# Optimization experiments

Hardware: AMD Instinct MI355X
Metric: run time of the kernel (lower is better)

Reference implementation:

```python
import jax, jax.numpy as jnp
import numpy as np
from jax import lax


def _conv(x, w, b):
    out = lax.conv_general_dilated(x, w, (1, 1), [(0, 0), (0, 0)],
                                   dimension_numbers=('NCHW', 'OIHW', 'NCHW'))
    return out + b[None, :, None, None]


def _bn(x, g, b, eps=1e-5):
    # BatchNorm2d in training mode: biased batch statistics over (N,H,W)
    m = jnp.mean(x, axis=(0, 2, 3), keepdims=True)
    v = jnp.var(x, axis=(0, 2, 3), keepdims=True)
    return (x - m) * lax.rsqrt(v + eps) * g[None, :, None, None] + b[None, :, None, None]


def _maxpool2(x):
    return lax.reduce_window(x, -jnp.inf, lax.max, (1, 1, 2, 2), (1, 1, 2, 2), 'VALID')


def _topk_mask(x, k):
    # TopK module: keep the k largest-|.| channels per (b,h,w), zero the rest.
    a = jnp.abs(x)
    kth = lax.top_k(jnp.moveaxis(a, 1, -1), k)[0][..., -1]  # [B,H,W] k-th largest |x|
    return x * (a >= kth[:, None, :, :]).astype(x.dtype)


def _embiggen(x):
    # im2col 3x3 stride 1 valid, flattened channel-major (c, kh, kw) like
    # patch.contiguous().view(B,-1) in the torch loop, but fully vectorized.
    B, C, H, W = x.shape
    Ho, Wo = H - 2, W - 2
    patches = jnp.stack([x[:, :, i:i + Ho, j:j + Wo]
                         for i in range(3) for j in range(3)], axis=2)  # [B,C,9,Ho,Wo]
    return patches.reshape(B, C * 9, Ho, Wo)


def setup_inputs() -> dict:
    key = jax.random.key(0)
    ks = jax.random.split(key, 40)
    it = iter(range(40))

    def w(shape):
        fan_in = int(np.prod(shape[1:]))
        return (jax.random.normal(ks[next(it)], shape, jnp.float32)
                / np.float32(np.sqrt(fan_in)))

    def bias(n):
        return jax.random.normal(ks[next(it)], (n,), jnp.float32) * 0.01

    def gamma(n):
        return jax.random.uniform(ks[next(it)], (n,), jnp.float32, 0.5, 1.5)

    inp = {}
    inp['x'] = jax.random.normal(ks[next(it)], (256, 3, 32, 32), jnp.float32)
    inp['enc_w'] = w((256, 3, 3, 3)); inp['enc_b'] = bias(256)
    inp['dec_w'] = w((27, 256, 1, 1)); inp['dec_b'] = bias(27)
    inp['red_w'] = w((64, 256, 1, 1)); inp['red_b'] = bias(64)
    inp['bn1_g'] = gamma(64); inp['bn1_b'] = bias(64)
    inp['conv1_w'] = w((96, 64, 3, 3)); inp['conv1_b'] = bias(96)
    inp['bn2_g'] = gamma(96); inp['bn2_b'] = bias(96)
    inp['conv2_w'] = w((128, 96, 3, 3)); inp['conv2_b'] = bias(128)
    inp['bn3_g'] = gamma(128); inp['bn3_b'] = bias(128)
    inp['conv3_w'] = w((160, 128, 3, 3)); inp['conv3_b'] = bias(160)
    inp['bn4_g'] = gamma(160); inp['bn4_b'] = bias(160)
    inp['conv4_w'] = w((192, 160, 3, 3)); inp['conv4_b'] = bias(192)
    inp['bn5_g'] = gamma(192); inp['bn5_b'] = bias(192)
    inp['conv5_w'] = w((256, 192, 3, 3)); inp['conv5_b'] = bias(256)
    inp['bnc_g'] = gamma(256); inp['bnc_b'] = bias(256)
    inp['fc_w'] = w((100, 1024)); inp['fc_b'] = bias(100)
    inp['k'] = 32  # round(64 / k_div=2)
    return inp


def reference(x, enc_w, enc_b, dec_w, dec_b, red_w, red_b,
              bn1_g, bn1_b, conv1_w, conv1_b,
              bn2_g, bn2_b, conv2_w, conv2_b,
              bn3_g, bn3_b, conv3_w, conv3_b,
              bn4_g, bn4_b, conv4_w, conv4_b,
              bn5_g, bn5_b, conv5_w, conv5_b,
              bnc_g, bnc_b, fc_w, fc_b, k):
    # SparseCodingLayer_First (encoder+topk computed once; torch recomputes identically)
    s = _topk_mask(_conv(x, enc_w, enc_b), k)            # [B,256,30,30]
    dec = jax.nn.sigmoid(_conv(s, dec_w, dec_b))         # [B,27,30,30]
    target = lax.stop_gradient(_embiggen(x))             # detached im2col target
    aux_loss = jnp.mean((target - dec) ** 2)
    h = _conv(s, red_w, red_b)                           # [B,64,30,30]
    # Conv6 backbone
    h = _maxpool2(_conv(jax.nn.relu(_bn(h, bn1_g, bn1_b)), conv1_w, conv1_b))  # [B,96,14,14]
    h = _conv(jax.nn.relu(_bn(h, bn2_g, bn2_b)), conv2_w, conv2_b)             # [B,128,12,12]
    h = _conv(jax.nn.relu(_bn(h, bn3_g, bn3_b)), conv3_w, conv3_b)             # [B,160,10,10]
    h = _maxpool2(_conv(jax.nn.relu(_bn(h, bn4_g, bn4_b)), conv4_w, conv4_b))  # [B,192,4,4]
    h = _conv(jax.nn.relu(_bn(h, bn5_g, bn5_b)), conv5_w, conv5_b)             # [B,256,2,2]
    feat = lax.stop_gradient(h)  # usecase == 'pretrain': features detached
    f = _bn(feat, bnc_g, bnc_b).reshape(feat.shape[0], -1)  # [B,1024]
    logits = f @ fc_w.T + fc_b                               # [B,100]
    preds = jnp.argmax(logits, axis=1)
    return logits, preds, aux_loss
```

## Files before the change

### kernel.cpp

```cpp
#include <hip/hip_runtime.h>

#define DEV_INLINE __device__ __forceinline__
typedef unsigned long long ull;
typedef unsigned int u32;
typedef unsigned short u16;
typedef __attribute__((ext_vector_type(8))) short short8v;
typedef __attribute__((ext_vector_type(4))) float f32x4;

DEV_INLINE u32 rne16(float f){
  u32 u = __float_as_uint(f);
  return (u + 0x7fffu + ((u>>16)&1u)) >> 16;
}
DEV_INLINE u32 packsplit(float a){
  u32 h = rne16(a);
  float hf = __uint_as_float(h<<16);
  u32 l = rne16(a - hf);
  return h | (l<<16);
}
DEV_INLINE float unpackv(u32 w){
  return __uint_as_float(w<<16) + __uint_as_float(w & 0xffff0000u);
}

__global__ void prep_all(const float* __restrict__ enc_w, float* __restrict__ encTg,
                         const float* __restrict__ dec_w, float* __restrict__ decT,
                         const float* __restrict__ red_w, float* __restrict__ redT,
                         const float* __restrict__ fc_w,  float* __restrict__ fcT,
                         const float* __restrict__ c1w, u16* __restrict__ W1h, u16* __restrict__ W1l,
                         const float* __restrict__ c2w, u16* __restrict__ W2h, u16* __restrict__ W2l,
                         const float* __restrict__ c3w, u16* __restrict__ W3h, u16* __restrict__ W3l,
                         const float* __restrict__ c4w, u16* __restrict__ W4h, u16* __restrict__ W4l,
                         const float* __restrict__ c5w, u16* __restrict__ W5h, u16* __restrict__ W5l)
{
  const int b = blockIdx.x, t = threadIdx.x;
  auto t2 = [&](const float* A, float* AT, int R, int C, int base){
    int i = (b-base)*256 + t; if (i < R*C){ int r=i%R, c=i/R; AT[i] = A[r*C+c]; }
  };
  auto pk = [&](const float* W, u16* wh, u16* wl, int CIN, int COUT, int base){
    int TPI = CIN/32;
    int eid = (b-base)*256 + t;
    if (eid >= 9*TPI*COUT*32) return;
    int kl = eid & 31;
    int rem = eid >> 5;
    int co = rem % COUT, ks = rem / COUT;
    int tap = ks/TPI, cib = (ks - tap*TPI)*32;
    float w = W[((size_t)(co*CIN + cib + kl))*9 + tap];
    u32 h = rne16(w);
    float hf = __uint_as_float(h<<16);
    u32 l = rne16(w - hf);
    wh[(size_t)rem*32 + kl] = (u16)h;
    wl[(size_t)rem*32 + kl] = (u16)l;
  };
  if      (b < 27)   t2(enc_w, encTg, 256, 27, 0);
  else if (b < 54)   t2(dec_w, decT, 27, 256, 27);
  else if (b < 118)  t2(red_w, redT, 64, 256, 54);
  else if (b < 518)  t2(fc_w,  fcT, 100, 1024, 118);
  else if (b < 734)  pk(c1w, W1h, W1l, 64, 96, 518);
  else if (b < 1166) pk(c2w, W2h, W2l, 96, 128, 734);
  else if (b < 1886) pk(c3w, W3h, W3l, 128, 160, 1166);
  else if (b < 2966) pk(c4w, W4h, W4l, 160, 192, 1886);
  else               pk(c5w, W5h, W5l, 192, 256, 2966);
}

__global__ __launch_bounds__(256, 4) void stage_a1(
    const float* __restrict__ encTg, const float* __restrict__ enc_b,
    const float* __restrict__ x, const int* __restrict__ kp,
    float* __restrict__ svg_v, unsigned char* __restrict__ svg_i)
{
  __shared__ float  rows[9*32];
  __shared__ float  svf[30*33];
  __shared__ unsigned char svi[30*33];

  const int t = threadIdx.x, oh = blockIdx.x, b = blockIdx.y;
  const int k = __builtin_amdgcn_readfirstlane(*kp);
  const int wid = t>>6, lane = t&63;
  const float4* encW4 = (const float4*)encTg;

  for (int e=t; e<288; e+=256){
    int ci = e/96, r = (e/32)%3, xx = e&31;
    rows[(ci*3+r)*32+xx] = x[((b*3+ci)*32 + (oh+r))*32 + xx];
  }
  for (int e=t; e<990; e+=256){ svf[e]=0.f; svi[e]=0; }
  __syncthreads();

  const float4 eb = ((const float4*)enc_b)[lane];

  auto cnt4 = [&](unsigned c, unsigned u0, unsigned u1, unsigned u2, unsigned u3)->int{
    return __popcll(__ballot(u0>=c)) + __popcll(__ballot(u1>=c))
         + __popcll(__ballot(u2>=c)) + __popcll(__ballot(u3>=c));
  };
  auto compact = [&](float v0,float v1,float v2,float v3,
                     unsigned u0,unsigned u1,unsigned u2,unsigned u3,
                     unsigned th, int pi){
    bool k0=u0>=th, k1=u1>=th, k2=u2>=th, k3=u3>=th;
    ull B0=__ballot(k0), B1=__ballot(k1), B2=__ballot(k2), B3=__ballot(k3);
    ull below=(1ull<<lane)-1ull;
    int n0=__popcll(B0), n1=__popcll(B1), n2=__popcll(B2);
    int o0=__popcll(B0&below);
    int o1=n0+__popcll(B1&below);
    int o2=n0+n1+__popcll(B2&below);
    int o3=n0+n1+n2+__popcll(B3&below);
    float* sf = &svf[pi*33]; unsigned char* si = &svi[pi*33];
    if (k0&&o0<32){ sf[o0]=v0; si[o0]=(unsigned char)(4*lane+0); }
    if (k1&&o1<32){ sf[o1]=v1; si[o1]=(unsigned char)(4*lane+1); }
    if (k2&&o2<32){ sf[o2]=v2; si[o2]=(unsigned char)(4*lane+2); }
    if (k3&&o3<32){ sf[o3]=v3; si[o3]=(unsigned char)(4*lane+3); }
  };

  for (int it=0; it<4; ++it){
    const int pr = wid*4 + it;
    if (pr >= 15) break;
    const int ow0 = 2*pr;

    float a0=eb.x,a1=eb.y,a2=eb.z,a3=eb.w;
    float c0=eb.x,c1=eb.y,c2=eb.z,c3=eb.w;
    #pragma unroll
    for (int ci=0; ci<3; ++ci)
      #pragma unroll
      for (int i=0;i<3;++i){
        const int rbase = (ci*3+i)*32 + ow0;
        float p0 = rows[rbase+0], p1 = rows[rbase+1];
        float p2 = rows[rbase+2], p3 = rows[rbase+3];
        float4 w0 = encW4[(ci*9+i*3+0)*64 + lane];
        float4 w1 = encW4[(ci*9+i*3+1)*64 + lane];
        float4 w2 = encW4[(ci*9+i*3+2)*64 + lane];
        a0=fmaf(w0.x,p0,a0); a1=fmaf(w0.y,p0,a1); a2=fmaf(w0.z,p0,a2); a3=fmaf(w0.w,p0,a3);
        c0=fmaf(w0.x,p1,c0); c1=fmaf(w0.y,p1,c1); c2=fmaf(w0.z,p1,c2); c3=fmaf(w0.w,p1,c3);
        a0=fmaf(w1.x,p1,a0); a1=fmaf(w1.y,p1,a1); a2=fmaf(w1.z,p1,a2); a3=fmaf(w1.w,p1,a3);
        c0=fmaf(w1.x,p2,c0); c1=fmaf(w1.y,p2,c1); c2=fmaf(w1.z,p2,c2); c3=fmaf(w1.w,p2,c3);
        a0=fmaf(w2.x,p2,a0); a1=fmaf(w2.y,p2,a1); a2=fmaf(w2.z,p2,a2); a3=fmaf(w2.w,p2,a3);
        c0=fmaf(w2.x,p3,c0); c1=fmaf(w2.y,p3,c1); c2=fmaf(w2.z,p3,c2); c3=fmaf(w2.w,p3,c3);
      }

    unsigned A0=__float_as_uint(a0)&0x7fffffffu, A1=__float_as_uint(a1)&0x7fffffffu;
    unsigned A2=__float_as_uint(a2)&0x7fffffffu, A3=__float_as_uint(a3)&0x7fffffffu;
    unsigned C0=__float_as_uint(c0)&0x7fffffffu, C1=__float_as_uint(c1)&0x7fffffffu;
    unsigned C2=__float_as_uint(c2)&0x7fffffffu, C3=__float_as_uint(c3)&0x7fffffffu;

    unsigned thA=0, thB=0;
    int dA=0, dB=0;
    for (int bit=30; bit>=0; --bit){
      if (!dA){
        unsigned c = thA | (1u<<bit);
        int n = cnt4(c,A0,A1,A2,A3);
        if (n>=k) thA=c;
        if (n==k) dA=1;
      }
      if (!dB){
        unsigned c = thB | (1u<<bit);
        int n = cnt4(c,C0,C1,C2,C3);
        if (n>=k) thB=c;
        if (n==k) dB=1;
      }
      if (dA & dB) break;
    }

    compact(a0,a1,a2,a3, A0,A1,A2,A3, thA, ow0);
    compact(c0,c1,c2,c3, C0,C1,C2,C3, thB, ow0+1);
  }
  __syncthreads();

  const size_t gbase = (size_t)b*900 + (size_t)oh*30;
  for (int e=t; e<960; e+=256){
    int jj = e/30, pi = e - jj*30;
    svg_v[(size_t)jj*230400 + gbase + pi] = svf[pi*33+jj];
    svg_i[(size_t)jj*230400 + gbase + pi] = svi[pi*33+jj];
  }
}

__global__ __launch_bounds__(256, 2) void stage_a2(
    const float* __restrict__ svg_v, const unsigned char* __restrict__ svg_i,
    const float* __restrict__ decT, const float* __restrict__ dec_b,
    const float* __restrict__ x, float* __restrict__ auxp)
{
  __shared__ __align__(16) float decl[256*28];
  __shared__ float redbuf[256];
  const int t = threadIdx.x;
  for (int e=t; e<6912; e+=256){
    int r = e/27, o = e - r*27;
    decl[r*28+o] = decT[e];
  }
  __syncthreads();

  const int pos = blockIdx.x*256 + t;
  const int b = pos/900, rem = pos - b*900;
  const int oh = rem/30, ow = rem - (rem/30)*30;

  float d[27];
  #pragma unroll
  for (int o=0;o<27;++o) d[o] = dec_b[o];
  for (int jj=0; jj<32; ++jj){
    float v  = svg_v[(size_t)jj*230400 + pos];
    int  idx = (int)svg_i[(size_t)jj*230400 + pos];
    const float4* wr4 = (const float4*)(decl + idx*28);
    float4 w0=wr4[0], w1=wr4[1], w2=wr4[2], w3=wr4[3], w4=wr4[4], w5=wr4[5], w6=wr4[6];
    d[0]=fmaf(v,w0.x,d[0]);  d[1]=fmaf(v,w0.y,d[1]);  d[2]=fmaf(v,w0.z,d[2]);  d[3]=fmaf(v,w0.w,d[3]);
    d[4]=fmaf(v,w1.x,d[4]);  d[5]=fmaf(v,w1.y,d[5]);  d[6]=fmaf(v,w1.z,d[6]);  d[7]=fmaf(v,w1.w,d[7]);
    d[8]=fmaf(v,w2.x,d[8]);  d[9]=fmaf(v,w2.y,d[9]);  d[10]=fmaf(v,w2.z,d[10]); d[11]=fmaf(v,w2.w,d[11]);
    d[12]=fmaf(v,w3.x,d[12]); d[13]=fmaf(v,w3.y,d[13]); d[14]=fmaf(v,w3.z,d[14]); d[15]=fmaf(v,w3.w,d[15]);
    d[16]=fmaf(v,w4.x,d[16]); d[17]=fmaf(v,w4.y,d[17]); d[18]=fmaf(v,w4.z,d[18]); d[19]=fmaf(v,w4.w,d[19]);
    d[20]=fmaf(v,w5.x,d[20]); d[21]=fmaf(v,w5.y,d[21]); d[22]=fmaf(v,w5.z,d[22]); d[23]=fmaf(v,w5.w,d[23]);
    d[24]=fmaf(v,w6.x,d[24]); d[25]=fmaf(v,w6.y,d[25]); d[26]=fmaf(v,w6.z,d[26]);
  }
  float acc = 0.f;
  #pragma unroll
  for (int o=0;o<27;++o){
    int ci = o/9, r2 = (o - ci*9)/3, c2 = o%3;
    float tg = x[((b*3+ci)*32 + (oh+r2))*32 + (ow+c2)];
    float dv = 1.f/(1.f + __expf(-d[o]));
    float df = tg - dv;
    acc = fmaf(df, df, acc);
  }
  redbuf[t]=acc; __syncthreads();
  for (int off=128; off; off>>=1){ if (t<off) redbuf[t]+=redbuf[t+off]; __syncthreads(); }
  if (t==0) auxp[blockIdx.x] = redbuf[0];
}

__global__ __launch_bounds__(256) void stage_a3p2(
    const float* __restrict__ svg_v, const unsigned char* __restrict__ svg_i,
    const float* __restrict__ redT, const float* __restrict__ red_b,
    u32* __restrict__ x1p, float* __restrict__ psum1, float* __restrict__ psq1)
{
  __shared__ __align__(16) float redl[256*68];
  __shared__ u32   obuf[256*65];
  const int t = threadIdx.x;
  for (int e=t; e<16384; e+=256) redl[(e>>6)*68 + (e&63)] = redT[e];
  __syncthreads();

  const int pos = blockIdx.x*256 + t;

  float v[32]; int a[32];
  #pragma unroll
  for (int j=0;j<32;++j) v[j] = svg_v[(size_t)j*230400 + pos];
  #pragma unroll
  for (int j=0;j<32;++j) a[j] = (int)svg_i[(size_t)j*230400 + pos]*17;

  const float4* redl4 = (const float4*)redl;
  #pragma unroll 2
  for (int ocb=0; ocb<16; ++ocb){
    float s0 = red_b[4*ocb+0], s1 = red_b[4*ocb+1];
    float s2 = red_b[4*ocb+2], s3 = red_b[4*ocb+3];
    #pragma unroll
    for (int j=0;j<32;++j){
      float4 w = redl4[a[j] + ocb];
      s0 = fmaf(v[j], w.x, s0); s1 = fmaf(v[j], w.y, s1);
      s2 = fmaf(v[j], w.z, s2); s3 = fmaf(v[j], w.w, s3);
    }
    obuf[t*65 + 4*ocb+0] = packsplit(s0);
    obuf[t*65 + 4*ocb+1] = packsplit(s1);
    obuf[t*65 + 4*ocb+2] = packsplit(s2);
    obuf[t*65 + 4*ocb+3] = packsplit(s3);
  }
  __syncthreads();

  const size_t base = (size_t)blockIdx.x*16384;
  float s = 0.f, q = 0.f;
  for (int e=t; e<16384; e+=256){
    u32 w = obuf[(e>>6)*65 + (e&63)];
    x1p[base + e] = w;
    float vv = unpackv(w);
    s += vv; q = fmaf(vv, vv, q);
  }
  float* ls = redl; float* lq = redl + 256;
  ls[t] = s; lq[t] = q; __syncthreads();
  if (t < 128){ ls[t] += ls[t+128]; lq[t] += lq[t+128]; } __syncthreads();
  if (t < 64){
    psum1[(size_t)blockIdx.x*64 + t] = ls[t] + ls[t+64];
    psq1 [(size_t)blockIdx.x*64 + t] = lq[t] + lq[t+64];
  }
}

__global__ __launch_bounds__(256) void bn1_final(
    const float* __restrict__ ps, const float* __restrict__ pq,
    const float* __restrict__ g, const float* __restrict__ b2,
    float* __restrict__ sc, float* __restrict__ sh)
{
  __shared__ float ls[256], lq[256];
  const int c = blockIdx.x, t = threadIdx.x;
  float s=0.f, q=0.f;
  for (int i=t; i<900; i+=256){ s += ps[(size_t)i*64+c]; q += pq[(size_t)i*64+c]; }
  ls[t]=s; lq[t]=q; __syncthreads();
  for (int off=128; off; off>>=1){
    if (t<off){ ls[t]+=ls[t+off]; lq[t]+=lq[t+off]; } __syncthreads();
  }
  if (t==0){
    constexpr float inv_n = 1.f/230400.f;
    float m = ls[0]*inv_n;
    float var = fmaf(lq[0], inv_n, -m*m);
    float rs = rsqrtf(var + 1e-5f);
    float scale = g[c]*rs;
    sc[c] = scale;
    sh[c] = fmaf(-m, scale, b2[c]);
  }
}

template<int C>
__global__ __launch_bounds__(256) void bn_finalG(
    const float* __restrict__ ps, const float* __restrict__ pq, int G,
    const float* __restrict__ g, const float* __restrict__ b2,
    float* __restrict__ sc, float* __restrict__ sh, float inv_n)
{
  __shared__ float ls[256], lq[256];
  const int c = blockIdx.x, t = threadIdx.x;
  float s=0.f, q=0.f;
  for (int i=t; i<G; i+=256){ s += ps[(size_t)i*C+c]; q += pq[(size_t)i*C+c]; }
  ls[t]=s; lq[t]=q; __syncthreads();
  for (int off=128; off; off>>=1){
    if (t<off){ ls[t]+=ls[t+off]; lq[t]+=lq[t+off]; } __syncthreads();
  }
  if (t==0){
    float m = ls[0]*inv_n;
    float var = fmaf(lq[0], inv_n, -m*m);
    float rs = rsqrtf(var + 1e-5f);
    float scale = g[c]*rs;
    sc[c] = scale;
    sh[c] = fmaf(-m, scale, b2[c]);
  }
}

template<int C>
__global__ void cvt_repack(u32* __restrict__ xp, const float* __restrict__ sc,
                           const float* __restrict__ sh, int total4){
  int i = blockIdx.x*256 + threadIdx.x;
  if (i >= total4) return;
  uint4* p = (uint4*)xp;
  uint4 w = p[i];
  int cb = (i*4) % C;
  w.x = packsplit(fmaxf(fmaf(unpackv(w.x), sc[cb+0], sh[cb+0]), 0.f));
  w.y = packsplit(fmaxf(fmaf(unpackv(w.y), sc[cb+1], sh[cb+1]), 0.f));
  w.z = packsplit(fmaxf(fmaf(unpackv(w.z), sc[cb+2], sh[cb+2]), 0.f));
  w.w = packsplit(fmaxf(fmaf(unpackv(w.w), sc[cb+3], sh[cb+3]), 0.f));
  p[i] = w;
}

template<int CIN,int COUT,int HIN,int WIN,int BM,int MW,bool POOL,bool PKOUT>
__global__ __launch_bounds__(256) void conv_mfma(
    const u32* __restrict__ xp, const u16* __restrict__ wh,
    const u16* __restrict__ wl, const float* __restrict__ bias,
    void* __restrict__ y_, float* __restrict__ psC, float* __restrict__ qsC)
{
  constexpr int HC=HIN-2, WC=WIN-2, TPI=CIN/32, KS=9*TPI, NCH=COUT/16;
  const int t = threadIdx.x, wid = t>>6, lane = t&63;
  const int p0 = blockIdx.x*BM;
  const int colg = lane>>4;
  const int col = lane&15;
  float* yf = (float*)y_;
  u32*   yp = (u32*)y_;

  const u32* Aptr[MW];
  #pragma unroll
  for (int m=0;m<MW;++m){
    int l = (wid*MW+m)*16 + col;
    int lc = l < BM ? l : BM-1;
    int p = p0 + lc;
    int b = p/(HC*WC); int rem = p - b*(HC*WC);
    int oh = rem/WC, ow = rem - (rem/WC)*WC;
    Aptr[m] = xp + ((size_t)((b*HIN+oh)*WIN+ow))*CIN + colg*8;
  }
  const size_t wb = (size_t)col*32 + colg*8;

  f32x4 acc[MW][NCH];
  #pragma unroll
  for (int m=0;m<MW;++m)
    #pragma unroll
    for (int nc=0;nc<NCH;++nc) acc[m][nc] = (f32x4){0.f,0.f,0.f,0.f};

  for (int ks=0; ks<KS; ++ks){
    const int tap = ks/TPI, cib = (ks - tap*TPI)*32;
    const int kh = tap/3, kw = tap - kh*3;
    short8v ah[MW], al[MW];
    #pragma unroll
    for (int m=0;m<MW;++m){
      const u32* ap = Aptr[m] + (kh*WIN + kw)*CIN + cib;
      uint4 qa = *(const uint4*)(ap);
      uint4 qb = *(const uint4*)(ap+4);
      ah[m][0]=(short)(qa.x&0xffffu); al[m][0]=(short)(qa.x>>16);
      ah[m][1]=(short)(qa.y&0xffffu); al[m][1]=(short)(qa.y>>16);
      ah[m][2]=(short)(qa.z&0xffffu); al[m][2]=(short)(qa.z>>16);
      ah[m][3]=(short)(qa.w&0xffffu); al[m][3]=(short)(qa.w>>16);
      ah[m][4]=(short)(qb.x&0xffffu); al[m][4]=(short)(qb.x>>16);
      ah[m][5]=(short)(qb.y&0xffffu); al[m][5]=(short)(qb.y>>16);
      ah[m][6]=(short)(qb.z&0xffffu); al[m][6]=(short)(qb.z>>16);
      ah[m][7]=(short)(qb.w&0xffffu); al[m][7]=(short)(qb.w>>16);
    }
    const u16* whp = wh + (size_t)ks*COUT*32 + wb;
    const u16* wlp = wl + (size_t)ks*COUT*32 + wb;
    #pragma unroll
    for (int nc=0;nc<NCH;++nc){
      short8v bh = *(const short8v*)(whp + nc*512);
      short8v bl = *(const short8v*)(wlp + nc*512);
      #pragma unroll
      for (int m=0;m<MW;++m){
        acc[m][nc] = __builtin_amdgcn_mfma_f32_16x16x32_bf16(ah[m], bh, acc[m][nc], 0,0,0);
        acc[m][nc] = __builtin_amdgcn_mfma_f32_16x16x32_bf16(ah[m], bl, acc[m][nc], 0,0,0);
        acc[m][nc] = __builtin_amdgcn_mfma_f32_16x16x32_bf16(al[m], bh, acc[m][nc], 0,0,0);
      }
    }
  }

  if constexpr (!POOL){
    __shared__ float ldsS[4][COUT], ldsQ[4][COUT];
    float sacc[NCH], qacc[NCH];
    #pragma unroll
    for (int nc=0;nc<NCH;++nc){ sacc[nc]=0.f; qacc[nc]=0.f; }
    #pragma unroll
    for (int m=0;m<MW;++m){
      const int lr0 = (wid*MW+m)*16 + colg*4;
      #pragma unroll
      for (int nc=0;nc<NCH;++nc){
        float bv = bias[nc*16+col];
        #pragma unroll
        for (int r=0;r<4;++r)
          if (lr0+r < BM){
            float ov = acc[m][nc][r] + bv;
            float vv;
            if constexpr (PKOUT){
              u32 w = packsplit(ov);
              yp[(size_t)(p0+lr0+r)*COUT + nc*16+col] = w;
              vv = unpackv(w);
            } else {
              yf[(size_t)(p0+lr0+r)*COUT + nc*16+col] = ov;
              vv = ov;
            }
            sacc[nc] += vv; qacc[nc] = fmaf(vv, vv, qacc[nc]);
          }
      }
    }
    #pragma unroll
    for (int nc=0;nc<NCH;++nc){
      float s_ = sacc[nc], q_ = qacc[nc];
      s_ += __shfl_xor(s_, 16); q_ += __shfl_xor(q_, 16);
      s_ += __shfl_xor(s_, 32); q_ += __shfl_xor(q_, 32);
      if (colg == 0){ ldsS[wid][nc*16+col] = s_; ldsQ[wid][nc*16+col] = q_; }
    }
    __syncthreads();
    if (t < COUT){
      psC[(size_t)blockIdx.x*COUT + t] = ldsS[0][t]+ldsS[1][t]+ldsS[2][t]+ldsS[3][t];
      qsC[(size_t)blockIdx.x*COUT + t] = ldsQ[0][t]+ldsQ[1][t]+ldsQ[2][t]+ldsQ[3][t];
    }
  } else {
    constexpr int LDC = COUT+4;
    __shared__ float lds[BM*LDC];
    #pragma unroll
    for (int m=0;m<MW;++m){
      const int lr0 = (wid*MW+m)*16 + colg*4;
      #pragma unroll
      for (int nc=0;nc<NCH;++nc){
        float bv = bias[nc*16+col];
        #pragma unroll
        for (int r=0;r<4;++r)
          if (lr0+r < BM) lds[(lr0+r)*LDC + nc*16+col] = acc[m][nc][r] + bv;
      }
    }
    __syncthreads();
    constexpr int WPO = WC/2;
    const size_t pbase = (size_t)p0/4;
    if (t < COUT){
      float s = 0.f, q = 0.f;
      for (int pl=0; pl<BM/4; ++pl){
        int poh = pl / WPO, pw = pl - poh*WPO;
        int r = (2*poh)*WC + 2*pw;
        float mx = fmaxf(fmaxf(lds[r*LDC+t],      lds[(r+1)*LDC+t]),
                         fmaxf(lds[(r+WC)*LDC+t], lds[(r+WC+1)*LDC+t]));
        float vv;
        if constexpr (PKOUT){
          u32 w = packsplit(mx);
          yp[(pbase + pl)*COUT + t] = w;
          vv = unpackv(w);
        } else {
          yf[(pbase + pl)*COUT + t] = mx;
          vv = mx;
        }
        s += vv; q = fmaf(vv, vv, q);
      }
      psC[(size_t)blockIdx.x*COUT + t] = s;
      qsC[(size_t)blockIdx.x*COUT + t] = q;
    }
  }
}

__global__ __launch_bounds__(256) void fc_kernel(
    const float* __restrict__ a5, const float* __restrict__ scale, const float* __restrict__ shift,
    const float* __restrict__ fcT, const float* __restrict__ fc_b,
    const float* __restrict__ auxp, float* __restrict__ outp)
{
  const int b = blockIdx.x, t = threadIdx.x;
  if (b == 256){
    __shared__ float s[256];
    float a=0.f;
    for (int i=t; i<900; i+=256) a += auxp[i];
    s[t]=a; __syncthreads();
    for (int off=128; off; off>>=1){ if (t<off) s[t]+=s[t+off]; __syncthreads(); }
    if (t==0) outp[25856] = s[0] / 6220800.0f;
    return;
  }
  __shared__ float f[1024];
  __shared__ float part[256];
  __shared__ float lg[128];
  for (int e=t; e<1024; e+=256){
    int c = e & 255, hw = e >> 8;
    float v = a5[b*1024 + e];
    f[c*4 + hw] = fmaf(v, scale[c], shift[c]);
  }
  __syncthreads();
  const int o = t & 127, half = t >> 7;
  float s = 0.f;
  if (o < 100){
    const float* fp = f + half*512;
    const float* wp = fcT + half*512*100 + o;
    for (int j=0;j<512;++j) s = fmaf(fp[j], wp[j*100], s);
  }
  part[t] = s; __syncthreads();
  if (t < 128){
    float logit = part[t] + part[t+128] + ((t<100)? fc_b[t] : 0.f);
    lg[t] = (t<100)? logit : -3.0e38f;
    if (t<100) outp[b*100 + t] = logit;
  }
  __syncthreads();
  if (t==0){
    float m = lg[0]; int mi = 0;
    for (int i=1;i<100;++i){ if (lg[i] > m){ m = lg[i]; mi = i; } }
    outp[25600 + b] = (float)mi;
  }
}

extern "C" void kernel_launch(void* const* d_in, const int* in_sizes, int n_in,
                              void* d_out, int out_size, void* d_ws, size_t ws_size,
                              hipStream_t stream)
{
  (void)in_sizes; (void)n_in; (void)out_size;
  const float* x     = (const float*)d_in[0];
  const float* enc_w = (const float*)d_in[1];
  const float* enc_b = (const float*)d_in[2];
  const float* dec_w = (const float*)d_in[3];
  const float* dec_b = (const float*)d_in[4];
  const float* red_w = (const float*)d_in[5];
  const float* red_b = (const float*)d_in[6];
  const float* bn1_g = (const float*)d_in[7];  const float* bn1_b = (const float*)d_in[8];
  const float* c1w   = (const float*)d_in[9];  const float* c1b   = (const float*)d_in[10];
  const float* bn2_g = (const float*)d_in[11]; const float* bn2_b = (const float*)d_in[12];
  const float* c2w   = (const float*)d_in[13]; const float* c2b   = (const float*)d_in[14];
  const float* bn3_g = (const float*)d_in[15]; const float* bn3_b = (const float*)d_in[16];
  const float* c3w   = (const float*)d_in[17]; const float* c3b   = (const float*)d_in[18];
  const float* bn4_g = (const float*)d_in[19]; const float* bn4_b = (const float*)d_in[20];
  const float* c4w   = (const float*)d_in[21]; const float* c4b   = (const float*)d_in[22];
  const float* bn5_g = (const float*)d_in[23]; const float* bn5_b = (const float*)d_in[24];
  const float* c5w   = (const float*)d_in[25]; const float* c5b   = (const float*)d_in[26];
  const float* bnc_g = (const float*)d_in[27]; const float* bnc_b = (const float*)d_in[28];
  const float* fc_w  = (const float*)d_in[29]; const float* fc_b  = (const float*)d_in[30];
  const int*   kp    = (const int*)d_in[31];
  float* out = (float*)d_out;
  float* ws  = (float*)d_ws;

  constexpr size_t OFF_ENCT = 0;
  constexpr size_t OFF_DECT = 7168;
  constexpr size_t OFF_REDT = 14336;
  constexpr size_t OFF_FCT  = 30720;
  constexpr size_t OFF_W1H = 133120, OFF_W1L = 160768;
  constexpr size_t OFF_W2H = 188416, OFF_W2L = 243712;
  constexpr size_t OFF_W3H = 299008, OFF_W3L = 391168;
  constexpr size_t OFF_W4H = 483328, OFF_W4L = 621568;
  constexpr size_t OFF_W5H = 759808, OFF_W5L = 980992;
  constexpr size_t OFF_SS1 = 1202176, OFF_SS2 = 1202304, OFF_SS3 = 1202496;
  constexpr size_t OFF_SS4 = 1202752, OFF_SS5 = 1203072, OFF_SSC = 1203456;
  constexpr size_t OFF_AUX  = 1302272;
  constexpr size_t OFF_B    = 1303296;
  constexpr size_t OFF_C    = 16048896;
  constexpr size_t OFF_P1S  = 25264896;
  constexpr size_t OFF_P1Q  = OFF_P1S + 57600;
  constexpr size_t OFF_PCS  = OFF_P1Q + 57600;
  constexpr size_t OFF_PCQ  = OFF_PCS + 172032;
  constexpr size_t TOTALF   = OFF_PCQ + 172032;
  if (ws_size < TOTALF*sizeof(float)) return;

  float* encTg = ws + OFF_ENCT;
  float* decT = ws + OFF_DECT; float* redT = ws + OFF_REDT; float* fcT = ws + OFF_FCT;
  u16* W1h = (u16*)(ws+OFF_W1H); u16* W1l = (u16*)(ws+OFF_W1L);
  u16* W2h = (u16*)(ws+OFF_W2H); u16* W2l = (u16*)(ws+OFF_W2L);
  u16* W3h = (u16*)(ws+OFF_W3H); u16* W3l = (u16*)(ws+OFF_W3L);
  u16* W4h = (u16*)(ws+OFF_W4H); u16* W4l = (u16*)(ws+OFF_W4L);
  u16* W5h = (u16*)(ws+OFF_W5H); u16* W5l = (u16*)(ws+OFF_W5L);
  float* ss1 = ws+OFF_SS1; float* ss2 = ws+OFF_SS2; float* ss3 = ws+OFF_SS3;
  float* ss4 = ws+OFF_SS4; float* ss5 = ws+OFF_SS5; float* ssc = ws+OFF_SSC;
  float* auxp = ws+OFF_AUX;
  float* psum1 = ws+OFF_P1S; float* psq1 = ws+OFF_P1Q;
  float* pcs = ws+OFF_PCS;  float* pcq = ws+OFF_PCQ;
  u32*   x1p = (u32*)(ws+OFF_B);
  u32*   y2p = (u32*)(ws+OFF_B);
  u32*   p4p = (u32*)(ws+OFF_B);
  float* svv = ws+OFF_C;
  unsigned char* svi = (unsigned char*)(ws+OFF_C+7372800);
  u32*   p1p = (u32*)(ws+OFF_C);
  u32*   y3p = (u32*)(ws+OFF_C);
  float* y5  = ws+OFF_C;

  prep_all<<<4694, 256, 0, stream>>>(enc_w, encTg, dec_w, decT, red_w, redT, fc_w, fcT,
                                     c1w, W1h, W1l, c2w, W2h, W2l, c3w, W3h, W3l,
                                     c4w, W4h, W4l, c5w, W5h, W5l);

  stage_a1<<<dim3(30,256), 256, 0, stream>>>(encTg, enc_b, x, kp, svv, svi);
  stage_a2<<<900, 256, 0, stream>>>(svv, svi, decT, dec_b, x, auxp);
  stage_a3p2<<<900, 256, 0, stream>>>(svv, svi, redT, red_b, x1p, psum1, psq1);

  bn1_final<<<64, 256, 0, stream>>>(psum1, psq1, bn1_g, bn1_b, ss1, ss1+64);
  cvt_repack<64><<<14400, 256, 0, stream>>>(x1p, ss1, ss1+64, 3686400);

  conv_mfma<64,96,30,30,112,2,true,true><<<1792, 256, 0, stream>>>(x1p, W1h, W1l, c1b, p1p, pcs, pcq);
  bn_finalG<96><<<96, 256, 0, stream>>>(pcs, pcq, 1792, bn2_g, bn2_b, ss2, ss2+96, 1.f/50176.f);
  cvt_repack<96><<<(1204224+255)/256, 256, 0, stream>>>(p1p, ss2, ss2+96, 1204224);

  conv_mfma<96,128,14,14,192,3,false,true><<<192, 256, 0, stream>>>(p1p, W2h, W2l, c2b, y2p, pcs, pcq);
  bn_finalG<128><<<128, 256, 0, stream>>>(pcs, pcq, 192, bn3_g, bn3_b, ss3, ss3+128, 1.f/36864.f);
  cvt_repack<128><<<(1179648+255)/256, 256, 0, stream>>>(y2p, ss3, ss3+128, 1179648);

  conv_mfma<128,160,12,12,128,2,false,true><<<200, 256, 0, stream>>>(y2p, W3h, W3l, c3b, y3p, pcs, pcq);
  bn_finalG<160><<<160, 256, 0, stream>>>(pcs, pcq, 200, bn4_g, bn4_b, ss4, ss4+160, 1.f/25600.f);
  cvt_repack<160><<<(1024000+255)/256, 256, 0, stream>>>(y3p, ss4, ss4+160, 1024000);

  conv_mfma<160,192,10,10,64,1,true,true><<<256, 256, 0, stream>>>(y3p, W4h, W4l, c4b, p4p, pcs, pcq);
  bn_finalG<192><<<192, 256, 0, stream>>>(pcs, pcq, 256, bn5_g, bn5_b, ss5, ss5+192, 1.f/4096.f);
  cvt_repack<192><<<(196608+255)/256, 256, 0, stream>>>(p4p, ss5, ss5+192, 196608);

  conv_mfma<192,256,4,4,64,1,false,false><<<16, 256, 0, stream>>>(p4p, W5h, W5l, c5b, y5, pcs, pcq);
  bn_finalG<256><<<256, 256, 0, stream>>>(pcs, pcq, 16, bnc_g, bnc_b, ssc, ssc+256, 1.f/1024.f);
  fc_kernel<<<257, 256, 0, stream>>>(y5, ssc, ssc+256, fcT, fc_b, auxp, out);
}
```

Measured before the change: 1.096 ms.

## Fuse decoder aux-loss and reducer conv kernels to share sparse input loads

Merges the decoder/aux-loss kernel into the reducer 1x1 conv kernel so the top-k sparse values and indices are read from global memory once instead of twice. The decoder weights are now pre-padded to a 28-float stride by prep_all and read directly from global memory (likely cache-resident) instead of being staged in LDS. The cost is one fewer launch and less global traffic, in exchange for higher register pressure in the fused kernel (32 values, 32 indices, 27 accumulators) and uncoalesced gather reads of decoder weights from global memory.

```diff
diff --git a/kernel.cpp b/kernel.cpp
--- a/kernel.cpp
+++ b/kernel.cpp
@@ -22,7 +22,7 @@
 }
 
 __global__ void prep_all(const float* __restrict__ enc_w, float* __restrict__ encTg,
-                         const float* __restrict__ dec_w, float* __restrict__ decT,
+                         const float* __restrict__ dec_w, float* __restrict__ decT28,
                          const float* __restrict__ red_w, float* __restrict__ redT,
                          const float* __restrict__ fc_w,  float* __restrict__ fcT,
                          const float* __restrict__ c1w, u16* __restrict__ W1h, u16* __restrict__ W1l,
@@ -51,7 +51,10 @@
     wl[(size_t)rem*32 + kl] = (u16)l;
   };
   if      (b < 27)   t2(enc_w, encTg, 256, 27, 0);
-  else if (b < 54)   t2(dec_w, decT, 27, 256, 27);
+  else if (b < 54){
+    int i = (b-27)*256 + t;
+    if (i < 6912){ int o = i%27, idx = i/27; decT28[idx*28+o] = dec_w[o*256+idx]; }
+  }
   else if (b < 118)  t2(red_w, redT, 64, 256, 54);
   else if (b < 518)  t2(fc_w,  fcT, 100, 1024, 118);
   else if (b < 734)  pk(c1w, W1h, W1l, 64, 96, 518);
@@ -167,72 +170,60 @@
   }
 }
 
-__global__ __launch_bounds__(256, 2) void stage_a2(
+__global__ __launch_bounds__(256) void stage_a23(
     const float* __restrict__ svg_v, const unsigned char* __restrict__ svg_i,
-    const float* __restrict__ decT, const float* __restrict__ dec_b,
-    const float* __restrict__ x, float* __restrict__ auxp)
-{
-  __shared__ __align__(16) float decl[256*28];
+    const float* __restrict__ redT, const float* __restrict__ red_b,
+    const float* __restrict__ decT28, const float* __restrict__ dec_b,
+    const float* __restrict__ x,
+    u32* __restrict__ x1p, float* __restrict__ psum1, float* __restrict__ psq1,
+    float* __restrict__ auxp)
+{
+  __shared__ __align__(16) float redl[256*68];
+  __shared__ u32   obuf[256*65];
   __shared__ float redbuf[256];
   const int t = threadIdx.x;
-  for (int e=t; e<6912; e+=256){
-    int r = e/27, o = e - r*27;
-    decl[r*28+o] = decT[e];
-  }
+  for (int e=t; e<16384; e+=256) redl[(e>>6)*68 + (e&63)] = redT[e];
   __syncthreads();
 
   const int pos = blockIdx.x*256 + t;
   const int b = pos/900, rem = pos - b*900;
   const int oh = rem/30, ow = rem - (rem/30)*30;
-
-  float d[27];
-  #pragma unroll
-  for (int o=0;o<27;++o) d[o] = dec_b[o];
-  for (int jj=0; jj<32; ++jj){
-    float v  = svg_v[(size_t)jj*230400 + pos];
-    int  idx = (int)svg_i[(size_t)jj*230400 + pos];
-    const float4* wr4 = (const float4*)(decl + idx*28);
-    float4 w0=wr4[0], w1=wr4[1], w2=wr4[2], w3=wr4[3], w4=wr4[4], w5=wr4[5], w6=wr4[6];
-    d[0]=fmaf(v,w0.x,d[0]);  d[1]=fmaf(v,w0.y,d[1]);  d[2]=fmaf(v,w0.z,d[2]);  d[3]=fmaf(v,w0.w,d[3]);
-    d[4]=fmaf(v,w1.x,d[4]);  d[5]=fmaf(v,w1.y,d[5]);  d[6]=fmaf(v,w1.z,d[6]);  d[7]=fmaf(v,w1.w,d[7]);
-    d[8]=fmaf(v,w2.x,d[8]);  d[9]=fmaf(v,w2.y,d[9]);  d[10]=fmaf(v,w2.z,d[10]); d[11]=fmaf(v,w2.w,d[11]);
-    d[12]=fmaf(v,w3.x,d[12]); d[13]=fmaf(v,w3.y,d[13]); d[14]=fmaf(v,w3.z,d[14]); d[15]=fmaf(v,w3.w,d[15]);
-    d[16]=fmaf(v,w4.x,d[16]); d[17]=fmaf(v,w4.y,d[17]); d[18]=fmaf(v,w4.z,d[18]); d[19]=fmaf(v,w4.w,d[19]);
-    d[20]=fmaf(v,w5.x,d[20]); d[21]=fmaf(v,w5.y,d[21]); d[22]=fmaf(v,w5.z,d[22]); d[23]=fmaf(v,w5.w,d[23]);
-    d[24]=fmaf(v,w6.x,d[24]); d[25]=fmaf(v,w6.y,d[25]); d[26]=fmaf(v,w6.z,d[26]);
-  }
-  float acc = 0.f;
-  #pragma unroll
-  for (int o=0;o<27;++o){
-    int ci = o/9, r2 = (o - ci*9)/3, c2 = o%3;
-    float tg = x[((b*3+ci)*32 + (oh+r2))*32 + (ow+c2)];
-    float dv = 1.f/(1.f + __expf(-d[o]));
-    float df = tg - dv;
-    acc = fmaf(df, df, acc);
-  }
-  redbuf[t]=acc; __syncthreads();
-  for (int off=128; off; off>>=1){ if (t<off) redbuf[t]+=redbuf[t+off]; __syncthreads(); }
-  if (t==0) auxp[blockIdx.x] = redbuf[0];
-}
-
-__global__ __launch_bounds__(256) void stage_a3p2(
-    const float* __restrict__ svg_v, const unsigned char* __restrict__ svg_i,
-    const float* __restrict__ redT, const float* __restrict__ red_b,
-    u32* __restrict__ x1p, float* __restrict__ psum1, float* __restrict__ psq1)
-{
-  __shared__ __align__(16) float redl[256*68];
-  __shared__ u32   obuf[256*65];
-  const int t = threadIdx.x;
-  for (int e=t; e<16384; e+=256) redl[(e>>6)*68 + (e&63)] = redT[e];
-  __syncthreads();
-
-  const int pos = blockIdx.x*256 + t;
 
   float v[32]; int a[32];
   #pragma unroll
   for (int j=0;j<32;++j) v[j] = svg_v[(size_t)j*230400 + pos];
   #pragma unroll
-  for (int j=0;j<32;++j) a[j] = (int)svg_i[(size_t)j*230400 + pos]*17;
+  for (int j=0;j<32;++j) a[j] = (int)svg_i[(size_t)j*230400 + pos];
+
+  {
+    float d[27];
+    #pragma unroll
+    for (int o=0;o<27;++o) d[o] = dec_b[o];
+    for (int jj=0; jj<32; ++jj){
+      float vv = v[jj];
+      const float4* wr4 = (const float4*)(decT28 + a[jj]*28);
+      float4 w0=wr4[0], w1=wr4[1], w2=wr4[2], w3=wr4[3], w4=wr4[4], w5=wr4[5], w6=wr4[6];
+      d[0]=fmaf(vv,w0.x,d[0]);  d[1]=fmaf(vv,w0.y,d[1]);  d[2]=fmaf(vv,w0.z,d[2]);  d[3]=fmaf(vv,w0.w,d[3]);
+      d[4]=fmaf(vv,w1.x,d[4]);  d[5]=fmaf(vv,w1.y,d[5]);  d[6]=fmaf(vv,w1.z,d[6]);  d[7]=fmaf(vv,w1.w,d[7]);
+      d[8]=fmaf(vv,w2.x,d[8]);  d[9]=fmaf(vv,w2.y,d[9]);  d[10]=fmaf(vv,w2.z,d[10]); d[11]=fmaf(vv,w2.w,d[11]);
+      d[12]=fmaf(vv,w3.x,d[12]); d[13]=fmaf(vv,w3.y,d[13]); d[14]=fmaf(vv,w3.z,d[14]); d[15]=fmaf(vv,w3.w,d[15]);
+      d[16]=fmaf(vv,w4.x,d[16]); d[17]=fmaf(vv,w4.y,d[17]); d[18]=fmaf(vv,w4.z,d[18]); d[19]=fmaf(vv,w4.w,d[19]);
+      d[20]=fmaf(vv,w5.x,d[20]); d[21]=fmaf(vv,w5.y,d[21]); d[22]=fmaf(vv,w5.z,d[22]); d[23]=fmaf(vv,w5.w,d[23]);
+      d[24]=fmaf(vv,w6.x,d[24]); d[25]=fmaf(vv,w6.y,d[25]); d[26]=fmaf(vv,w6.z,d[26]);
+    }
+    float acc = 0.f;
+    #pragma unroll
+    for (int o=0;o<27;++o){
+      int ci = o/9, r2 = (o - ci*9)/3, c2 = o%3;
+      float tg = x[((b*3+ci)*32 + (oh+r2))*32 + (ow+c2)];
+      float dv = 1.f/(1.f + __expf(-d[o]));
+      float df = tg - dv;
+      acc = fmaf(df, df, acc);
+    }
+    redbuf[t]=acc; __syncthreads();
+    for (int off=128; off; off>>=1){ if (t<off) redbuf[t]+=redbuf[t+off]; __syncthreads(); }
+    if (t==0) auxp[blockIdx.x] = redbuf[0];
+  }
 
   const float4* redl4 = (const float4*)redl;
   #pragma unroll 2
@@ -241,7 +232,7 @@
     float s2 = red_b[4*ocb+2], s3 = red_b[4*ocb+3];
     #pragma unroll
     for (int j=0;j<32;++j){
-      float4 w = redl4[a[j] + ocb];
+      float4 w = redl4[a[j]*17 + ocb];
       s0 = fmaf(v[j], w.x, s0); s1 = fmaf(v[j], w.y, s1);
       s2 = fmaf(v[j], w.z, s2); s3 = fmaf(v[j], w.w, s3);
     }
@@ -573,7 +564,7 @@
   if (ws_size < TOTALF*sizeof(float)) return;
 
   float* encTg = ws + OFF_ENCT;
-  float* decT = ws + OFF_DECT; float* redT = ws + OFF_REDT; float* fcT = ws + OFF_FCT;
+  float* decT28 = ws + OFF_DECT; float* redT = ws + OFF_REDT; float* fcT = ws + OFF_FCT;
   u16* W1h = (u16*)(ws+OFF_W1H); u16* W1l = (u16*)(ws+OFF_W1L);
   u16* W2h = (u16*)(ws+OFF_W2H); u16* W2l = (u16*)(ws+OFF_W2L);
   u16* W3h = (u16*)(ws+OFF_W3H); u16* W3l = (u16*)(ws+OFF_W3L);
@@ -593,13 +584,13 @@
   u32*   y3p = (u32*)(ws+OFF_C);
   float* y5  = ws+OFF_C;
 
-  prep_all<<<4694, 256, 0, stream>>>(enc_w, encTg, dec_w, decT, red_w, redT, fc_w, fcT,
+  prep_all<<<4694, 256, 0, stream>>>(enc_w, encTg, dec_w, decT28, red_w, redT, fc_w, fcT,
                                      c1w, W1h, W1l, c2w, W2h, W2l, c3w, W3h, W3l,
                                      c4w, W4h, W4l, c5w, W5h, W5l);
 
   stage_a1<<<dim3(30,256), 256, 0, stream>>>(encTg, enc_b, x, kp, svv, svi);
-  stage_a2<<<900, 256, 0, stream>>>(svv, svi, decT, dec_b, x, auxp);
-  stage_a3p2<<<900, 256, 0, stream>>>(svv, svi, redT, red_b, x1p, psum1, psq1);
+  stage_a23<<<900, 256, 0, stream>>>(svv, svi, redT, red_b, decT28, dec_b, x,
+                                     x1p, psum1, psq1, auxp);
 
   bn1_final<<<64, 256, 0, stream>>>(psum1, psq1, bn1_g, bn1_b, ss1, ss1+64);
   cvt_repack<64><<<14400, 256, 0, stream>>>(x1p, ss1, ss1+64, 3686400);
```

Result: slower. 1.130 ms (+3.1%).
